# Optimization experiments

Hardware: AMD Instinct MI355X
Metric: run time of the kernel (lower is better)

## Reference

```python
import jax, jax.numpy as jnp
import numpy as np

# Config matching TR_Conv(in_channels=128, out_channels=128, m=5, n=2, dilation=1,
#   concatenate=False -> G_add path, head_paramisloate=False, wide_erf=True, drop=0)
B, C_IN, T = 16, 128, 8192
C_OUT = 128
M, N = 5, 2
ZERO_NUM = 2               # floor(2**(N-1))
UNIT_FZ = 1 + ZERO_NUM     # 3
HEAD = ZERO_NUM            # head_paramisloate=False, zero_num>0 -> head = zero_num
GROUPS = HEAD              # G_add branch: groups = head, Pout_channels = out_channels
KERNEL = UNIT_FZ * (M - 1) + 1  # 13


def quick_gelu(x):
    return x * jax.nn.sigmoid(1.702 * x)


def pad_reflect_to(x, t):
    # TR_Conv.pad_num: reflect-pad last dim up to length t, split (d//2, d-d//2)
    d = t - x.shape[-1]
    if d <= 0:
        return x
    return jnp.pad(x, ((0, 0), (0, 0), (d // 2, d - d // 2)), mode='reflect')


def setup_inputs() -> dict:
    key = jax.random.key(0)
    k1, k2, k3 = jax.random.split(key, 3)
    x = jax.random.normal(k1, (B, C_IN, T), jnp.float32)
    fan_in = (C_IN // GROUPS) * KERNEL
    bound = 1.0 / np.sqrt(fan_in)
    w = jax.random.uniform(k2, (C_OUT, C_IN // GROUPS, KERNEL), jnp.float32, -bound, bound)
    b = jax.random.uniform(k3, (C_OUT,), jnp.float32, -bound, bound)
    return {"x": x, "w": w, "b": b}


def reference(x, w, b):
    t = x.shape[-1]
    # Zero-insertion (UNIT_FZ-1 zeros between samples) + Conv1d(kernel=13, pad=ZERO_NUM,
    # groups=2) expressed exactly via lhs_dilation (equivalent, avoids materializing zeros).
    out = jax.lax.conv_general_dilated(
        x, w, window_strides=(1,), padding=[(ZERO_NUM, ZERO_NUM)],
        lhs_dilation=(UNIT_FZ,), feature_group_count=GROUPS,
        dimension_numbers=('NCH', 'OIH', 'NCH'))  # [B, C_OUT, 3T-10]
    out = out + b[None, :, None]

    # x_m_mk: every UNIT_FZ-th output starting at UNIT_FZ-1, reflect-padded to T
    x_m_mk = pad_reflect_to(out[:, :, UNIT_FZ - 1::UNIT_FZ], t)  # [B, C_OUT, T]

    # wide_erf: sliding max over window M along time, zero-padded (floor/ceil of (M-1)/2)
    lp = (M - 1) // 2
    xp = jnp.pad(x_m_mk, ((0, 0), (0, 0), (lp, M - 1 - lp)))
    umax = jnp.max(jnp.stack([xp[:, :, k:k + t] for k in range(M)], 0), 0)  # [B,C_OUT,T]

    trimmed = out[:, :, :-UNIT_FZ]
    acc = jnp.zeros_like(x_m_mk)
    for j in range(ZERO_NUM):  # all_m=True path: r-l (gelu'd, G_add) and r+l terms
        r = pad_reflect_to(out[:, :, j + UNIT_FZ::UNIT_FZ], t)
        l = pad_reflect_to(trimmed[:, :, j::UNIT_FZ], t)
        minus = quick_gelu(r - l)          # G_add: gelu on the minus branch
        add = r + l
        base = (1.0 / HEAD) * x_m_mk + (1.0 / (2 * HEAD)) * umax  # drop(p=0) = identity
        acc = acc + (minus + base) + (add + base)
    # dilation=1: taylor_eq[:, :, 0::1] = sum over taylor_eq_list[1:]
    return acc
```

## Files before the change

kernel.cpp:

```cpp
#include <hip/hip_runtime.h>
#include <hip/hip_bf16.h>

typedef __attribute__((ext_vector_type(4))) float f32x4;
typedef __attribute__((ext_vector_type(8))) short bf16x8;
typedef unsigned short ushort_t;

#define T_LEN 8192
#define N_REFL 8187
#define TS 64
#define WIN 80
#define XW 88
#define POSTRIDE 66
#define PH_U16 (WIN * POSTRIDE)

__device__ __forceinline__ ushort_t f2bf(float f) {
    union { float f; unsigned u; } a; a.f = f;
    unsigned r = a.u + 0x7FFF + ((a.u >> 16) & 1);
    return (ushort_t)(r >> 16);
}

union bf2u { __hip_bfloat162 h; unsigned u; ushort_t s[2]; };

__device__ __forceinline__ unsigned pack_bf2(float a, float b) {
    bf2u x; x.h = __float22bfloat162_rn(make_float2(a, b));
    return x.u;
}
__device__ __forceinline__ float bflo(unsigned u) {
    union { unsigned u; float f; } x; x.u = u << 16; return x.f;
}
__device__ __forceinline__ float bfhi(unsigned u) {
    union { unsigned u; float f; } x; x.u = u & 0xffff0000u; return x.f;
}
__device__ __forceinline__ float qgelu(float d) {
    return __fdividef(d, 1.f + __expf(-1.702f * d));
}
__device__ __forceinline__ float rot_lane(float v, int byteIdx) {
    int r = __builtin_amdgcn_ds_bpermute(byteIdx, __builtin_bit_cast(int, v));
    return __builtin_bit_cast(float, r);
}

__global__ void convert_w_kernel(const float* __restrict__ w, ushort_t* __restrict__ wbf) {
    int idx = blockIdx.x * 256 + threadIdx.x;
    if (idx >= 128 * 64 * 13) return;
    int tap = idx % 13;
    int c   = (idx / 13) & 63;
    int o   = idx / (13 * 64);
    wbf[(tap * 128 + o) * 64 + c] = f2bf(w[idx]);
}

__global__ __launch_bounds__(256, 4)
void fused_trconv_kernel(const float* __restrict__ x, const ushort_t* __restrict__ wbf,
                         const float* __restrict__ bias, float* __restrict__ out) {
    __shared__ ushort_t smem[3 * PH_U16];
    ushort_t* xs = smem;

    const int bx    = blockIdx.x;
    const int tile  = bx & 127;
    const int g     = (bx >> 7) & 1;
    const int b     = bx >> 8;
    const int t0    = tile * TS;
    const int mbase = t0 - 8;
    const int tid   = threadIdx.x;

    const float* xg = x + ((size_t)b * 128 + (size_t)g * 64) * T_LEN;
    for (int cid = tid; cid < 64 * (XW / 4); cid += 256) {
        int c  = cid & 63;
        int kc = cid >> 6;
        int s0 = kc * 4;
        int m0 = mbase + s0;
        const float* src = xg + (size_t)c * T_LEN + m0;
        float v0, v1, v2, v3;
        if (m0 >= 0 && m0 + 3 < T_LEN) {
            float4 v = *(const float4*)src;
            v0 = v.x; v1 = v.y; v2 = v.z; v3 = v.w;
        } else {
            v0 = (m0 + 0 >= 0 && m0 + 0 < T_LEN) ? src[0] : 0.f;
            v1 = (m0 + 1 >= 0 && m0 + 1 < T_LEN) ? src[1] : 0.f;
            v2 = (m0 + 2 >= 0 && m0 + 2 < T_LEN) ? src[2] : 0.f;
            v3 = (m0 + 3 >= 0 && m0 + 3 < T_LEN) ? src[3] : 0.f;
        }
        unsigned p01 = pack_bf2(v0, v1);
        unsigned p23 = pack_bf2(v2, v3);
        xs[(s0 + 0) * 64 + (c ^ (((s0 + 0) & 7) << 3))] = (ushort_t)(p01 & 0xffff);
        xs[(s0 + 1) * 64 + (c ^ (((s0 + 1) & 7) << 3))] = (ushort_t)(p01 >> 16);
        xs[(s0 + 2) * 64 + (c ^ (((s0 + 2) & 7) << 3))] = (ushort_t)(p23 & 0xffff);
        xs[(s0 + 3) * 64 + (c ^ (((s0 + 3) & 7) << 3))] = (ushort_t)(p23 >> 16);
    }
    __syncthreads();

    const int lane = tid & 63;
    const int wv   = tid >> 6;
    const int row  = lane & 15;
    const int kb   = lane >> 4;

    f32x4 accA[5], accL0[5], accL1[5];
    #pragma unroll
    for (int q = 0; q < 5; ++q) {
        accA[q] = (f32x4){0.f, 0.f, 0.f, 0.f};
        accL0[q] = (f32x4){0.f, 0.f, 0.f, 0.f};
        accL1[q] = (f32x4){0.f, 0.f, 0.f, 0.f};
    }

    const int wo = g * 64 + wv * 16 + row;

    #pragma unroll
    for (int u = 0; u < 5; ++u) {
        #pragma unroll
        for (int h = 0; h < 2; ++h) {
            bf16x8 wf0 = *(const bf16x8*)(wbf + ((3 * u + 0) * 128 + wo) * 64 + h * 32 + kb * 8);
            bf16x8 wf1 = {}, wf2 = {};
            if (u < 4) {
                wf1 = *(const bf16x8*)(wbf + ((3 * u + 2) * 128 + wo) * 64 + h * 32 + kb * 8);
                wf2 = *(const bf16x8*)(wbf + ((3 * u + 1) * 128 + wo) * 64 + h * 32 + kb * 8);
            }
            #pragma unroll
            for (int q = 0; q < 5; ++q) {
                int s = 16 * q + row + u;
                const bf16x8 xa = *(const bf16x8*)(xs + s * 64 + ((h * 32 + kb * 8) ^ ((s & 7) << 3)));
                accA[q] = __builtin_amdgcn_mfma_f32_16x16x32_bf16(xa, wf0, accA[q], 0, 0, 0);
                if (u < 4) {
                    accL0[q] = __builtin_amdgcn_mfma_f32_16x16x32_bf16(xa, wf1, accL0[q], 0, 0, 0);
                    accL1[q] = __builtin_amdgcn_mfma_f32_16x16x32_bf16(xa, wf2, accL1[q], 0, 0, 0);
                }
            }
        }
    }
    const float bo = bias[wo];

    if (tile != 0 && tile != 127) {
        const int upIdx = ((lane + 16) & 63) << 2;
        const int dnIdx = ((lane + 48) & 63) << 2;

        float u0[6], u1[6], d2m[5], d3m[5], lu[6], lv[6];
        #pragma unroll
        for (int q = 0; q < 5; ++q) {
            u0[q] = rot_lane(accA[q][0], upIdx);
            u1[q] = rot_lane(accA[q][1], upIdx);
            d2m[q] = rot_lane(accA[q][2], dnIdx);
            d3m[q] = rot_lane(accA[q][3], dnIdx);
            lu[q] = rot_lane(accL0[q][0], upIdx);
            lv[q] = rot_lane(accL1[q][0], upIdx);
        }
        u0[5] = 0.f; u1[5] = 0.f; lu[5] = 0.f; lv[5] = 0.f;

        const bool kbLT3 = (kb < 3);
        const bool kbGT0 = (kb > 0);
        const float c7bo = 7.f * bo;
        float* outBase = out + ((size_t)(b * 128 + wo)) * T_LEN + (t0 - 6 + 4 * kb);

        #pragma unroll
        for (int q = 0; q < 5; ++q) {
            #pragma unroll
            for (int r = 0; r < 4; ++r) {
                float A0 = accA[q][r];
                float Ap1 = (r < 3) ? accA[q][r + 1] : (kbLT3 ? u0[q] : u0[q + 1]);
                float Ap2 = (r == 0) ? accA[q][2]
                          : (r == 1) ? accA[q][3]
                          : (r == 2) ? (kbLT3 ? u0[q] : u0[q + 1])
                                     : (kbLT3 ? u1[q] : u1[q + 1]);
                float Am1 = (r > 0) ? accA[q][r - 1]
                                    : (kbGT0 ? d3m[q] : (q > 0 ? d3m[q - 1] : 0.f));
                float Am2 = (r == 2) ? accA[q][0]
                          : (r == 3) ? accA[q][1]
                          : (r == 1) ? (kbGT0 ? d3m[q] : (q > 0 ? d3m[q - 1] : 0.f))
                                     : (kbGT0 ? d2m[q] : (q > 0 ? d2m[q - 1] : 0.f));
                float L0a = accL0[q][r];
                float L0b = (r < 3) ? accL0[q][r + 1] : (kbLT3 ? lu[q] : lu[q + 1]);
                float L1a = accL1[q][r];
                float L1b = (r < 3) ? accL1[q][r + 1] : (kbLT3 ? lv[q] : lv[q + 1]);

                float um = fmaxf(fmaxf(fmaxf(Am2, Am1), fmaxf(Ap1, Ap2)), A0);
                float res = 2.f * A0 + um + c7bo + (L0b + L0a) + (L1b + L1a)
                          + qgelu(L0b - L0a) + qgelu(L1b - L1a);

                bool ok = true;
                if (q == 0) ok = (4 * kb + r) >= 6;
                if (q == 4) ok = (4 * kb + r) <= 5;
                if (ok) outBase[16 * q + r] = res;
            }
        }
    } else {
        __syncthreads();
        #pragma unroll
        for (int q = 0; q < 5; ++q) {
            #pragma unroll
            for (int p = 0; p < 3; ++p) {
                const f32x4& a = (p == 0) ? accA[q] : (p == 1) ? accL0[q] : accL1[q];
                unsigned pa = pack_bf2(a[0] + bo, a[1] + bo);
                unsigned pb = pack_bf2(a[2] + bo, a[3] + bo);
                int base = p * PH_U16 + (16 * q + kb * 4) * POSTRIDE + wv * 16 + row;
                smem[base + 0 * POSTRIDE] = (ushort_t)(pa & 0xffff);
                smem[base + 1 * POSTRIDE] = (ushort_t)(pa >> 16);
                smem[base + 2 * POSTRIDE] = (ushort_t)(pb & 0xffff);
                smem[base + 3 * POSTRIDE] = (ushort_t)(pb >> 16);
            }
        }
        __syncthreads();

        const int tl = tid & 63;
        const int wq = tid >> 6;
        const int t  = t0 + tl;
        const ushort_t* phA  = smem;
        const ushort_t* phL0 = smem + PH_U16;
        const ushort_t* phL1 = smem + 2 * PH_U16;
        float* outp = out + ((size_t)b * 128 + (size_t)g * 64) * T_LEN + t;

        int  s5[5];
        bool in5[5];
        #pragma unroll
        for (int dt = 0; dt < 5; ++dt) {
            int tp = t + dt - 2;
            in5[dt] = ((unsigned)tp < (unsigned)T_LEN);
            int idx = tp - 2;
            idx = (idx < 0) ? -idx : idx;
            idx = (idx > N_REFL) ? (2 * N_REFL - idx) : idx;
            s5[dt] = idx - mbase;
        }
        const int sC = s5[2];
        for (int i = 0; i < 8; ++i) {
            int o = 2 * wq + 8 * i;
            unsigned av[5];
            #pragma unroll
            for (int dt = 0; dt < 5; ++dt)
                av[dt] = *(const unsigned*)(phA + s5[dt] * POSTRIDE + o);
            unsigned l0a = *(const unsigned*)(phL0 + (sC    ) * POSTRIDE + o);
            unsigned l0b = *(const unsigned*)(phL0 + (sC + 1) * POSTRIDE + o);
            unsigned l1a = *(const unsigned*)(phL1 + (sC    ) * POSTRIDE + o);
            unsigned l1b = *(const unsigned*)(phL1 + (sC + 1) * POSTRIDE + o);

            float xm_l = bflo(av[2]), xm_h = bfhi(av[2]);
            float um_l = -1e30f, um_h = -1e30f;
            #pragma unroll
            for (int dt = 0; dt < 5; ++dt) {
                um_l = fmaxf(um_l, in5[dt] ? bflo(av[dt]) : 0.f);
                um_h = fmaxf(um_h, in5[dt] ? bfhi(av[dt]) : 0.f);
            }
            float l0al = bflo(l0a), l0bl = bflo(l0b), l1al = bflo(l1a), l1bl = bflo(l1b);
            float l0ah = bfhi(l0a), l0bh = bfhi(l0b), l1ah = bfhi(l1a), l1bh = bfhi(l1b);

            float rl = 2.f * xm_l + um_l + (l0bl + l0al) + qgelu(l0bl - l0al)
                                         + (l1bl + l1al) + qgelu(l1bl - l1al);
            float rh = 2.f * xm_h + um_h + (l0bh + l0ah) + qgelu(l0bh - l0ah)
                                         + (l1bh + l1ah) + qgelu(l1bh - l1ah);
            outp[(size_t)(o    ) * T_LEN] = rl;
            outp[(size_t)(o + 1) * T_LEN] = rh;
        }
    }
}

extern "C" void kernel_launch(void* const* d_in, const int* in_sizes, int n_in,
                              void* d_out, int out_size, void* d_ws, size_t ws_size,
                              hipStream_t stream) {
    const float* x    = (const float*)d_in[0];
    const float* w    = (const float*)d_in[1];
    const float* bias = (const float*)d_in[2];
    float* out        = (float*)d_out;
    ushort_t* wbf     = (ushort_t*)d_ws;

    hipLaunchKernelGGL(convert_w_kernel, dim3(416), dim3(256), 0, stream, w, wbf);
    hipLaunchKernelGGL(fused_trconv_kernel, dim3(16 * 2 * 128), dim3(256), 0, stream,
                       x, wbf, bias, out);
}
```

Baseline: 94.36 us.

## Process four time tiles per block with shared x window, separate edge blocks

Interior blocks now cover 256 time steps: they stage one 288-sample bf16 x window in LDS and then run four 64-step sub-tiles over it. The reflect-boundary tiles move into 64 dedicated blocks at the end of the grid. This cuts the redundant halo loads and the per-block staging and barrier overhead, and removes the edge branch from interior blocks. In exchange the grid shrinks from 4096 to 1088 blocks, occupancy drops to 3 waves per SIMD, and weight fragments are re-read for each sub-tile.

```diff
diff --git a/kernel.cpp b/kernel.cpp
--- a/kernel.cpp
+++ b/kernel.cpp
@@ -7,11 +7,10 @@
 
 #define T_LEN 8192
 #define N_REFL 8187
-#define TS 64
-#define WIN 80
-#define XW 88
+#define GWIN 288
 #define POSTRIDE 66
-#define PH_U16 (WIN * POSTRIDE)
+#define PH_U16 (80 * POSTRIDE)
+#define N_INT 1024
 
 __device__ __forceinline__ ushort_t f2bf(float f) {
     union { float f; unsigned u; } a; a.f = f;
@@ -48,139 +47,213 @@
     wbf[(tap * 128 + o) * 64 + c] = f2bf(w[idx]);
 }
 
-__global__ __launch_bounds__(256, 4)
+__global__ __launch_bounds__(256, 3)
 void fused_trconv_kernel(const float* __restrict__ x, const ushort_t* __restrict__ wbf,
                          const float* __restrict__ bias, float* __restrict__ out) {
-    __shared__ ushort_t smem[3 * PH_U16];
-    ushort_t* xs = smem;
-
-    const int bx    = blockIdx.x;
-    const int tile  = bx & 127;
-    const int g     = (bx >> 7) & 1;
-    const int b     = bx >> 8;
-    const int t0    = tile * TS;
-    const int mbase = t0 - 8;
-    const int tid   = threadIdx.x;
-
-    const float* xg = x + ((size_t)b * 128 + (size_t)g * 64) * T_LEN;
-    for (int cid = tid; cid < 64 * (XW / 4); cid += 256) {
-        int c  = cid & 63;
-        int kc = cid >> 6;
-        int s0 = kc * 4;
-        int m0 = mbase + s0;
-        const float* src = xg + (size_t)c * T_LEN + m0;
-        float v0, v1, v2, v3;
-        if (m0 >= 0 && m0 + 3 < T_LEN) {
-            float4 v = *(const float4*)src;
-            v0 = v.x; v1 = v.y; v2 = v.z; v3 = v.w;
-        } else {
-            v0 = (m0 + 0 >= 0 && m0 + 0 < T_LEN) ? src[0] : 0.f;
-            v1 = (m0 + 1 >= 0 && m0 + 1 < T_LEN) ? src[1] : 0.f;
-            v2 = (m0 + 2 >= 0 && m0 + 2 < T_LEN) ? src[2] : 0.f;
-            v3 = (m0 + 3 >= 0 && m0 + 3 < T_LEN) ? src[3] : 0.f;
-        }
-        unsigned p01 = pack_bf2(v0, v1);
-        unsigned p23 = pack_bf2(v2, v3);
-        xs[(s0 + 0) * 64 + (c ^ (((s0 + 0) & 7) << 3))] = (ushort_t)(p01 & 0xffff);
-        xs[(s0 + 1) * 64 + (c ^ (((s0 + 1) & 7) << 3))] = (ushort_t)(p01 >> 16);
-        xs[(s0 + 2) * 64 + (c ^ (((s0 + 2) & 7) << 3))] = (ushort_t)(p23 & 0xffff);
-        xs[(s0 + 3) * 64 + (c ^ (((s0 + 3) & 7) << 3))] = (ushort_t)(p23 >> 16);
-    }
-    __syncthreads();
-
+    __shared__ ushort_t smem[GWIN * 64];
+
+    const int bx   = blockIdx.x;
+    const int tid  = threadIdx.x;
     const int lane = tid & 63;
     const int wv   = tid >> 6;
     const int row  = lane & 15;
     const int kb   = lane >> 4;
 
-    f32x4 accA[5], accL0[5], accL1[5];
-    #pragma unroll
-    for (int q = 0; q < 5; ++q) {
-        accA[q] = (f32x4){0.f, 0.f, 0.f, 0.f};
-        accL0[q] = (f32x4){0.f, 0.f, 0.f, 0.f};
-        accL1[q] = (f32x4){0.f, 0.f, 0.f, 0.f};
-    }
-
-    const int wo = g * 64 + wv * 16 + row;
-
-    #pragma unroll
-    for (int u = 0; u < 5; ++u) {
-        #pragma unroll
-        for (int h = 0; h < 2; ++h) {
-            bf16x8 wf0 = *(const bf16x8*)(wbf + ((3 * u + 0) * 128 + wo) * 64 + h * 32 + kb * 8);
-            bf16x8 wf1 = {}, wf2 = {};
-            if (u < 4) {
-                wf1 = *(const bf16x8*)(wbf + ((3 * u + 2) * 128 + wo) * 64 + h * 32 + kb * 8);
-                wf2 = *(const bf16x8*)(wbf + ((3 * u + 1) * 128 + wo) * 64 + h * 32 + kb * 8);
-            }
-            #pragma unroll
-            for (int q = 0; q < 5; ++q) {
-                int s = 16 * q + row + u;
-                const bf16x8 xa = *(const bf16x8*)(xs + s * 64 + ((h * 32 + kb * 8) ^ ((s & 7) << 3)));
-                accA[q] = __builtin_amdgcn_mfma_f32_16x16x32_bf16(xa, wf0, accA[q], 0, 0, 0);
-                if (u < 4) {
-                    accL0[q] = __builtin_amdgcn_mfma_f32_16x16x32_bf16(xa, wf1, accL0[q], 0, 0, 0);
-                    accL1[q] = __builtin_amdgcn_mfma_f32_16x16x32_bf16(xa, wf2, accL1[q], 0, 0, 0);
-                }
-            }
-        }
-    }
-    const float bo = bias[wo];
-
-    if (tile != 0 && tile != 127) {
+    if (bx < N_INT) {
+        const int go = bx & 31;
+        const int g  = (bx >> 5) & 1;
+        const int b  = bx >> 6;
+        const int mbase = 256 * go - 8;
+        const float* xg = x + ((size_t)b * 128 + (size_t)g * 64) * T_LEN;
+
+        {
+            const int cl = lane >> 2;
+            const int j  = lane & 3;
+            const int c  = wv * 16 + cl;
+            const float* src = xg + (size_t)c * T_LEN;
+            for (int it = 0; it < 18; ++it) {
+                int m0 = mbase + 16 * it + 4 * j;
+                float v0, v1, v2, v3;
+                if (m0 >= 0 && m0 + 3 < T_LEN) {
+                    float4 v = *(const float4*)(src + m0);
+                    v0 = v.x; v1 = v.y; v2 = v.z; v3 = v.w;
+                } else {
+                    v0 = ((unsigned)(m0 + 0) < (unsigned)T_LEN) ? src[m0 + 0] : 0.f;
+                    v1 = ((unsigned)(m0 + 1) < (unsigned)T_LEN) ? src[m0 + 1] : 0.f;
+                    v2 = ((unsigned)(m0 + 2) < (unsigned)T_LEN) ? src[m0 + 2] : 0.f;
+                    v3 = ((unsigned)(m0 + 3) < (unsigned)T_LEN) ? src[m0 + 3] : 0.f;
+                }
+                unsigned p01 = pack_bf2(v0, v1);
+                unsigned p23 = pack_bf2(v2, v3);
+                int w0 = 16 * it + 4 * j;
+                smem[(w0 + 0) * 64 + (c ^ (((w0 + 0) & 7) << 3))] = (ushort_t)(p01 & 0xffff);
+                smem[(w0 + 1) * 64 + (c ^ (((w0 + 1) & 7) << 3))] = (ushort_t)(p01 >> 16);
+                smem[(w0 + 2) * 64 + (c ^ (((w0 + 2) & 7) << 3))] = (ushort_t)(p23 & 0xffff);
+                smem[(w0 + 3) * 64 + (c ^ (((w0 + 3) & 7) << 3))] = (ushort_t)(p23 >> 16);
+            }
+        }
+        __syncthreads();
+
+        const int wo = g * 64 + wv * 16 + row;
+        const float bo = bias[wo];
+        const float c7bo = 7.f * bo;
         const int upIdx = ((lane + 16) & 63) << 2;
         const int dnIdx = ((lane + 48) & 63) << 2;
-
-        float u0[6], u1[6], d2m[5], d3m[5], lu[6], lv[6];
-        #pragma unroll
-        for (int q = 0; q < 5; ++q) {
-            u0[q] = rot_lane(accA[q][0], upIdx);
-            u1[q] = rot_lane(accA[q][1], upIdx);
-            d2m[q] = rot_lane(accA[q][2], dnIdx);
-            d3m[q] = rot_lane(accA[q][3], dnIdx);
-            lu[q] = rot_lane(accL0[q][0], upIdx);
-            lv[q] = rot_lane(accL1[q][0], upIdx);
-        }
-        u0[5] = 0.f; u1[5] = 0.f; lu[5] = 0.f; lv[5] = 0.f;
-
         const bool kbLT3 = (kb < 3);
         const bool kbGT0 = (kb > 0);
-        const float c7bo = 7.f * bo;
-        float* outBase = out + ((size_t)(b * 128 + wo)) * T_LEN + (t0 - 6 + 4 * kb);
-
+
+        #pragma unroll
+        for (int k = 0; k < 4; ++k) {
+            if ((go == 0 && k == 0) || (go == 31 && k == 3)) continue;
+            if (k) asm volatile("" ::: "memory");
+
+            f32x4 accA[5], accL0[5], accL1[5];
+            #pragma unroll
+            for (int q = 0; q < 5; ++q) {
+                accA[q]  = (f32x4){0.f, 0.f, 0.f, 0.f};
+                accL0[q] = (f32x4){0.f, 0.f, 0.f, 0.f};
+                accL1[q] = (f32x4){0.f, 0.f, 0.f, 0.f};
+            }
+
+            #pragma unroll
+            for (int u = 0; u < 5; ++u) {
+                #pragma unroll
+                for (int h = 0; h < 2; ++h) {
+                    bf16x8 wf0 = *(const bf16x8*)(wbf + ((3 * u + 0) * 128 + wo) * 64 + h * 32 + kb * 8);
+                    bf16x8 wf1 = {}, wf2 = {};
+                    if (u < 4) {
+                        wf1 = *(const bf16x8*)(wbf + ((3 * u + 2) * 128 + wo) * 64 + h * 32 + kb * 8);
+                        wf2 = *(const bf16x8*)(wbf + ((3 * u + 1) * 128 + wo) * 64 + h * 32 + kb * 8);
+                    }
+                    #pragma unroll
+                    for (int q = 0; q < 5; ++q) {
+                        int s = 64 * k + 16 * q + row + u;
+                        const bf16x8 xa = *(const bf16x8*)(smem + s * 64 + ((h * 32 + kb * 8) ^ ((s & 7) << 3)));
+                        accA[q] = __builtin_amdgcn_mfma_f32_16x16x32_bf16(xa, wf0, accA[q], 0, 0, 0);
+                        if (u < 4) {
+                            accL0[q] = __builtin_amdgcn_mfma_f32_16x16x32_bf16(xa, wf1, accL0[q], 0, 0, 0);
+                            accL1[q] = __builtin_amdgcn_mfma_f32_16x16x32_bf16(xa, wf2, accL1[q], 0, 0, 0);
+                        }
+                    }
+                }
+            }
+
+            float u0[6], u1[6], d2m[5], d3m[5], lu[6], lv[6];
+            #pragma unroll
+            for (int q = 0; q < 5; ++q) {
+                u0[q]  = rot_lane(accA[q][0], upIdx);
+                u1[q]  = rot_lane(accA[q][1], upIdx);
+                d2m[q] = rot_lane(accA[q][2], dnIdx);
+                d3m[q] = rot_lane(accA[q][3], dnIdx);
+                lu[q]  = rot_lane(accL0[q][0], upIdx);
+                lv[q]  = rot_lane(accL1[q][0], upIdx);
+            }
+            u0[5] = 0.f; u1[5] = 0.f; lu[5] = 0.f; lv[5] = 0.f;
+
+            const int t0k = 256 * go + 64 * k;
+            float* outBase = out + ((size_t)(b * 128 + wo)) * T_LEN + (t0k - 6 + 4 * kb);
+
+            #pragma unroll
+            for (int q = 0; q < 5; ++q) {
+                #pragma unroll
+                for (int r = 0; r < 4; ++r) {
+                    float A0 = accA[q][r];
+                    float Ap1 = (r < 3) ? accA[q][r + 1] : (kbLT3 ? u0[q] : u0[q + 1]);
+                    float Ap2 = (r == 0) ? accA[q][2]
+                              : (r == 1) ? accA[q][3]
+                              : (r == 2) ? (kbLT3 ? u0[q] : u0[q + 1])
+                                         : (kbLT3 ? u1[q] : u1[q + 1]);
+                    float Am1 = (r > 0) ? accA[q][r - 1]
+                                        : (kbGT0 ? d3m[q] : (q > 0 ? d3m[q - 1] : 0.f));
+                    float Am2 = (r == 2) ? accA[q][0]
+                              : (r == 3) ? accA[q][1]
+                              : (r == 1) ? (kbGT0 ? d3m[q] : (q > 0 ? d3m[q - 1] : 0.f))
+                                         : (kbGT0 ? d2m[q] : (q > 0 ? d2m[q - 1] : 0.f));
+                    float L0a = accL0[q][r];
+                    float L0b = (r < 3) ? accL0[q][r + 1] : (kbLT3 ? lu[q] : lu[q + 1]);
+                    float L1a = accL1[q][r];
+                    float L1b = (r < 3) ? accL1[q][r + 1] : (kbLT3 ? lv[q] : lv[q + 1]);
+
+                    float um = fmaxf(fmaxf(fmaxf(Am2, Am1), fmaxf(Ap1, Ap2)), A0);
+                    float res = 2.f * A0 + um + c7bo + (L0b + L0a) + (L1b + L1a)
+                              + qgelu(L0b - L0a) + qgelu(L1b - L1a);
+
+                    bool ok = true;
+                    if (q == 0) ok = (4 * kb + r) >= 6;
+                    if (q == 4) ok = (4 * kb + r) <= 5;
+                    if (ok) outBase[16 * q + r] = res;
+                }
+            }
+        }
+    } else {
+        const int idx  = bx - N_INT;
+        const int tile = (idx & 1) ? 127 : 0;
+        const int g    = (idx >> 1) & 1;
+        const int b    = idx >> 2;
+        const int t0    = tile * 64;
+        const int mbase = t0 - 8;
+        ushort_t* xs = smem;
+
+        const float* xg = x + ((size_t)b * 128 + (size_t)g * 64) * T_LEN;
+        for (int cid = tid; cid < 64 * 22; cid += 256) {
+            int c  = cid & 63;
+            int kc = cid >> 6;
+            int s0 = kc * 4;
+            int m0 = mbase + s0;
+            const float* src = xg + (size_t)c * T_LEN + m0;
+            float v0, v1, v2, v3;
+            if (m0 >= 0 && m0 + 3 < T_LEN) {
+                float4 v = *(const float4*)src;
+                v0 = v.x; v1 = v.y; v2 = v.z; v3 = v.w;
+            } else {
+                v0 = (m0 + 0 >= 0 && m0 + 0 < T_LEN) ? src[0] : 0.f;
+                v1 = (m0 + 1 >= 0 && m0 + 1 < T_LEN) ? src[1] : 0.f;
+                v2 = (m0 + 2 >= 0 && m0 + 2 < T_LEN) ? src[2] : 0.f;
+                v3 = (m0 + 3 >= 0 && m0 + 3 < T_LEN) ? src[3] : 0.f;
+            }
+            unsigned p01 = pack_bf2(v0, v1);
+            unsigned p23 = pack_bf2(v2, v3);
+            xs[(s0 + 0) * 64 + (c ^ (((s0 + 0) & 7) << 3))] = (ushort_t)(p01 & 0xffff);
+            xs[(s0 + 1) * 64 + (c ^ (((s0 + 1) & 7) << 3))] = (ushort_t)(p01 >> 16);
+            xs[(s0 + 2) * 64 + (c ^ (((s0 + 2) & 7) << 3))] = (ushort_t)(p23 & 0xffff);
+            xs[(s0 + 3) * 64 + (c ^ (((s0 + 3) & 7) << 3))] = (ushort_t)(p23 >> 16);
+        }
+        __syncthreads();
+
+        f32x4 accA[5], accL0[5], accL1[5];
         #pragma unroll
         for (int q = 0; q < 5; ++q) {
-            #pragma unroll
-            for (int r = 0; r < 4; ++r) {
-                float A0 = accA[q][r];
-                float Ap1 = (r < 3) ? accA[q][r + 1] : (kbLT3 ? u0[q] : u0[q + 1]);
-                float Ap2 = (r == 0) ? accA[q][2]
-                          : (r == 1) ? accA[q][3]
-                          : (r == 2) ? (kbLT3 ? u0[q] : u0[q + 1])
-                                     : (kbLT3 ? u1[q] : u1[q + 1]);
-                float Am1 = (r > 0) ? accA[q][r - 1]
-                                    : (kbGT0 ? d3m[q] : (q > 0 ? d3m[q - 1] : 0.f));
-                float Am2 = (r == 2) ? accA[q][0]
-                          : (r == 3) ? accA[q][1]
-                          : (r == 1) ? (kbGT0 ? d3m[q] : (q > 0 ? d3m[q - 1] : 0.f))
-                                     : (kbGT0 ? d2m[q] : (q > 0 ? d2m[q - 1] : 0.f));
-                float L0a = accL0[q][r];
-                float L0b = (r < 3) ? accL0[q][r + 1] : (kbLT3 ? lu[q] : lu[q + 1]);
-                float L1a = accL1[q][r];
-                float L1b = (r < 3) ? accL1[q][r + 1] : (kbLT3 ? lv[q] : lv[q + 1]);
-
-                float um = fmaxf(fmaxf(fmaxf(Am2, Am1), fmaxf(Ap1, Ap2)), A0);
-                float res = 2.f * A0 + um + c7bo + (L0b + L0a) + (L1b + L1a)
-                          + qgelu(L0b - L0a) + qgelu(L1b - L1a);
-
-                bool ok = true;
-                if (q == 0) ok = (4 * kb + r) >= 6;
-                if (q == 4) ok = (4 * kb + r) <= 5;
-                if (ok) outBase[16 * q + r] = res;
-            }
-        }
-    } else {
+            accA[q]  = (f32x4){0.f, 0.f, 0.f, 0.f};
+            accL0[q] = (f32x4){0.f, 0.f, 0.f, 0.f};
+            accL1[q] = (f32x4){0.f, 0.f, 0.f, 0.f};
+        }
+        const int wo = g * 64 + wv * 16 + row;
+
+        #pragma unroll
+        for (int u = 0; u < 5; ++u) {
+            #pragma unroll
+            for (int h = 0; h < 2; ++h) {
+                bf16x8 wf0 = *(const bf16x8*)(wbf + ((3 * u + 0) * 128 + wo) * 64 + h * 32 + kb * 8);
+                bf16x8 wf1 = {}, wf2 = {};
+                if (u < 4) {
+                    wf1 = *(const bf16x8*)(wbf + ((3 * u + 2) * 128 + wo) * 64 + h * 32 + kb * 8);
+                    wf2 = *(const bf16x8*)(wbf + ((3 * u + 1) * 128 + wo) * 64 + h * 32 + kb * 8);
+                }
+                #pragma unroll
+                for (int q = 0; q < 5; ++q) {
+                    int s = 16 * q + row + u;
+                    const bf16x8 xa = *(const bf16x8*)(xs + s * 64 + ((h * 32 + kb * 8) ^ ((s & 7) << 3)));
+                    accA[q] = __builtin_amdgcn_mfma_f32_16x16x32_bf16(xa, wf0, accA[q], 0, 0, 0);
+                    if (u < 4) {
+                        accL0[q] = __builtin_amdgcn_mfma_f32_16x16x32_bf16(xa, wf1, accL0[q], 0, 0, 0);
+                        accL1[q] = __builtin_amdgcn_mfma_f32_16x16x32_bf16(xa, wf2, accL1[q], 0, 0, 0);
+                    }
+                }
+            }
+        }
+        const float bo = bias[wo];
         __syncthreads();
+
         #pragma unroll
         for (int q = 0; q < 5; ++q) {
             #pragma unroll
@@ -211,10 +284,10 @@
         for (int dt = 0; dt < 5; ++dt) {
             int tp = t + dt - 2;
             in5[dt] = ((unsigned)tp < (unsigned)T_LEN);
-            int idx = tp - 2;
-            idx = (idx < 0) ? -idx : idx;
-            idx = (idx > N_REFL) ? (2 * N_REFL - idx) : idx;
-            s5[dt] = idx - mbase;
+            int ix = tp - 2;
+            ix = (ix < 0) ? -ix : ix;
+            ix = (ix > N_REFL) ? (2 * N_REFL - ix) : ix;
+            s5[dt] = ix - mbase;
         }
         const int sC = s5[2];
         for (int i = 0; i < 8; ++i) {
@@ -258,6 +331,6 @@
     ushort_t* wbf     = (ushort_t*)d_ws;
 
     hipLaunchKernelGGL(convert_w_kernel, dim3(416), dim3(256), 0, stream, w, wbf);
-    hipLaunchKernelGGL(fused_trconv_kernel, dim3(16 * 2 * 128), dim3(256), 0, stream,
+    hipLaunchKernelGGL(fused_trconv_kernel, dim3(N_INT + 64), dim3(256), 0, stream,
                        x, wbf, bias, out);
 }
```

Result: slower. 97.50 us (+3.3%).

## Fold neighbor-sum/difference into combined weights and split interior/boundary kernels

Applied to the files above, without the earlier changes.

Interior tiles now use precomputed combined weights so the MFMAs directly produce A, the full sum term (2A+L0+L0'+L1+L1'), and the two differences fed to quick_gelu. This removes the lane rotations and extra adds for the L terms in the epilogue, at the cost of four MFMA streams per tap instead of roughly three. Boundary tiles move to a separate small kernel, which removes branching from the interior kernel. The interior qgelu also switches to exp2 with a reciprocal.

```diff
diff --git a/kernel.cpp b/kernel.cpp
--- a/kernel.cpp
+++ b/kernel.cpp
@@ -7,11 +7,10 @@
 
 #define T_LEN 8192
 #define N_REFL 8187
-#define TS 64
-#define WIN 80
-#define XW 88
 #define POSTRIDE 66
-#define PH_U16 (WIN * POSTRIDE)
+#define PH_U16 (80 * POSTRIDE)
+#define N_INT 4032
+#define WS_WNEW_OFF 262144
 
 __device__ __forceinline__ ushort_t f2bf(float f) {
     union { float f; unsigned u; } a; a.f = f;
@@ -32,6 +31,9 @@
     union { unsigned u; float f; } x; x.u = u & 0xffff0000u; return x.f;
 }
 __device__ __forceinline__ float qgelu(float d) {
+    return d * __frcp_rn(1.f + exp2f(-2.4553418f * d));
+}
+__device__ __forceinline__ float qgelu2(float d) {
     return __fdividef(d, 1.f + __expf(-1.702f * d));
 }
 __device__ __forceinline__ float rot_lane(float v, int byteIdx) {
@@ -39,34 +41,166 @@
     return __builtin_bit_cast(float, r);
 }
 
-__global__ void convert_w_kernel(const float* __restrict__ w, ushort_t* __restrict__ wbf) {
+__global__ void convert_w_kernel(const float* __restrict__ w,
+                                 ushort_t* __restrict__ wold,
+                                 ushort_t* __restrict__ wnew) {
     int idx = blockIdx.x * 256 + threadIdx.x;
-    if (idx >= 128 * 64 * 13) return;
-    int tap = idx % 13;
-    int c   = (idx / 13) & 63;
-    int o   = idx / (13 * 64);
-    wbf[(tap * 128 + o) * 64 + c] = f2bf(w[idx]);
+    if (idx >= 8192) return;
+    int o = idx >> 6, c = idx & 63;
+    const float* wp = w + (size_t)idx * 13;
+    float t[13];
+    #pragma unroll
+    for (int k = 0; k < 13; ++k) t[k] = wp[k];
+    #pragma unroll
+    for (int k = 0; k < 13; ++k) wold[(k * 128 + o) * 64 + c] = f2bf(t[k]);
+    #pragma unroll
+    for (int k = 0; k < 5; ++k) {
+        float a   = t[3 * k];
+        float l0k = (k <= 3) ? t[3 * k + 2] : 0.f;
+        float l1k = (k <= 3) ? t[3 * k + 1] : 0.f;
+        float l0m = (k >= 1) ? t[3 * k - 1] : 0.f;
+        float l1m = (k >= 1) ? t[3 * k - 2] : 0.f;
+        wnew[((0 * 5 + k) * 128 + o) * 64 + c] = f2bf(a);
+        wnew[((1 * 5 + k) * 128 + o) * 64 + c] = f2bf(2.f * a + l0k + l0m + l1k + l1m);
+        wnew[((2 * 5 + k) * 128 + o) * 64 + c] = f2bf(l0m - l0k);
+        wnew[((3 * 5 + k) * 128 + o) * 64 + c] = f2bf(l1m - l1k);
+    }
+}
+
+__global__ __launch_bounds__(256, 3)
+void fused_int_kernel(const float* __restrict__ x, const ushort_t* __restrict__ wnew,
+                      const float* __restrict__ bias, float* __restrict__ out) {
+    __shared__ ushort_t xs[88 * 64];
+
+    const int bx   = blockIdx.x;
+    const int tid  = threadIdx.x;
+    const int lane = tid & 63;
+    const int wv   = tid >> 6;
+    const int row  = lane & 15;
+    const int kb   = lane >> 4;
+
+    const int gb   = bx / 126;
+    const int tile = 1 + (bx - gb * 126);
+    const int g    = gb & 1;
+    const int b    = gb >> 1;
+    const int t0   = tile * 64;
+    const int mbase = t0 - 8;
+
+    const float* xg = x + ((size_t)b * 128 + (size_t)g * 64) * T_LEN;
+    for (int cid = tid; cid < 64 * 22; cid += 256) {
+        int c  = cid & 63;
+        int s0 = (cid >> 6) * 4;
+        float4 v = *(const float4*)(xg + (size_t)c * T_LEN + (mbase + s0));
+        unsigned p01 = pack_bf2(v.x, v.y);
+        unsigned p23 = pack_bf2(v.z, v.w);
+        xs[(s0 + 0) * 64 + (c ^ (((s0 + 0) & 7) << 3))] = (ushort_t)(p01 & 0xffff);
+        xs[(s0 + 1) * 64 + (c ^ (((s0 + 1) & 7) << 3))] = (ushort_t)(p01 >> 16);
+        xs[(s0 + 2) * 64 + (c ^ (((s0 + 2) & 7) << 3))] = (ushort_t)(p23 & 0xffff);
+        xs[(s0 + 3) * 64 + (c ^ (((s0 + 3) & 7) << 3))] = (ushort_t)(p23 >> 16);
+    }
+    const int wo = g * 64 + wv * 16 + row;
+    const float bo = bias[wo];
+    __syncthreads();
+
+    f32x4 accA[5], accS[5], accD0[5], accD1[5];
+    #pragma unroll
+    for (int q = 0; q < 5; ++q) {
+        accA[q]  = (f32x4){0.f, 0.f, 0.f, 0.f};
+        accS[q]  = (f32x4){0.f, 0.f, 0.f, 0.f};
+        accD0[q] = (f32x4){0.f, 0.f, 0.f, 0.f};
+        accD1[q] = (f32x4){0.f, 0.f, 0.f, 0.f};
+    }
+
+    #pragma unroll
+    for (int u = 0; u < 5; ++u) {
+        #pragma unroll
+        for (int h = 0; h < 2; ++h) {
+            const int wbase = h * 32 + kb * 8;
+            bf16x8 wfA = *(const bf16x8*)(wnew + ((0 * 5 + u) * 128 + wo) * 64 + wbase);
+            bf16x8 wfS = *(const bf16x8*)(wnew + ((1 * 5 + u) * 128 + wo) * 64 + wbase);
+            bf16x8 wf0 = *(const bf16x8*)(wnew + ((2 * 5 + u) * 128 + wo) * 64 + wbase);
+            bf16x8 wf1 = *(const bf16x8*)(wnew + ((3 * 5 + u) * 128 + wo) * 64 + wbase);
+            #pragma unroll
+            for (int q = 0; q < 5; ++q) {
+                int s = 16 * q + row + u;
+                const bf16x8 xa = *(const bf16x8*)(xs + s * 64 + (wbase ^ ((s & 7) << 3)));
+                accA[q]  = __builtin_amdgcn_mfma_f32_16x16x32_bf16(xa, wfA, accA[q],  0, 0, 0);
+                accS[q]  = __builtin_amdgcn_mfma_f32_16x16x32_bf16(xa, wfS, accS[q],  0, 0, 0);
+                accD0[q] = __builtin_amdgcn_mfma_f32_16x16x32_bf16(xa, wf0, accD0[q], 0, 0, 0);
+                accD1[q] = __builtin_amdgcn_mfma_f32_16x16x32_bf16(xa, wf1, accD1[q], 0, 0, 0);
+            }
+        }
+    }
+
+    const int upIdx = ((lane + 16) & 63) << 2;
+    const int dnIdx = ((lane + 48) & 63) << 2;
+
+    float u0[6], u1[6], d2m[5], d3m[5];
+    #pragma unroll
+    for (int q = 0; q < 5; ++q) {
+        u0[q]  = rot_lane(accA[q][0], upIdx);
+        u1[q]  = rot_lane(accA[q][1], upIdx);
+        d2m[q] = rot_lane(accA[q][2], dnIdx);
+        d3m[q] = rot_lane(accA[q][3], dnIdx);
+    }
+    u0[5] = 0.f; u1[5] = 0.f;
+
+    const bool kbLT3 = (kb < 3);
+    const bool kbGT0 = (kb > 0);
+    const float c7bo = 7.f * bo;
+    float* outBase = out + ((size_t)(b * 128 + wo)) * T_LEN + (t0 - 6 + 4 * kb);
+
+    #pragma unroll
+    for (int q = 0; q < 5; ++q) {
+        #pragma unroll
+        for (int r = 0; r < 4; ++r) {
+            float A0 = accA[q][r];
+            float Ap1 = (r < 3) ? accA[q][r + 1] : (kbLT3 ? u0[q] : u0[q + 1]);
+            float Ap2 = (r == 0) ? accA[q][2]
+                      : (r == 1) ? accA[q][3]
+                      : (r == 2) ? (kbLT3 ? u0[q] : u0[q + 1])
+                                 : (kbLT3 ? u1[q] : u1[q + 1]);
+            float Am1 = (r > 0) ? accA[q][r - 1]
+                                : (kbGT0 ? d3m[q] : (q > 0 ? d3m[q - 1] : 0.f));
+            float Am2 = (r == 2) ? accA[q][0]
+                      : (r == 3) ? accA[q][1]
+                      : (r == 1) ? (kbGT0 ? d3m[q] : (q > 0 ? d3m[q - 1] : 0.f))
+                                 : (kbGT0 ? d2m[q] : (q > 0 ? d2m[q - 1] : 0.f));
+
+            float um  = fmaxf(fmaxf(fmaxf(Am2, Am1), A0), fmaxf(Ap1, Ap2));
+            float res = accS[q][r] + um + c7bo + qgelu(accD0[q][r]) + qgelu(accD1[q][r]);
+
+            bool ok = true;
+            if (q == 0) ok = (4 * kb + r) >= 6;
+            if (q == 4) ok = (4 * kb + r) <= 5;
+            if (ok) outBase[16 * q + r] = res;
+        }
+    }
 }
 
 __global__ __launch_bounds__(256, 4)
-void fused_trconv_kernel(const float* __restrict__ x, const ushort_t* __restrict__ wbf,
-                         const float* __restrict__ bias, float* __restrict__ out) {
+void fused_bnd_kernel(const float* __restrict__ x, const ushort_t* __restrict__ wbf,
+                      const float* __restrict__ bias, float* __restrict__ out) {
     __shared__ ushort_t smem[3 * PH_U16];
     ushort_t* xs = smem;
 
-    const int bx    = blockIdx.x;
-    const int tile  = bx & 127;
-    const int g     = (bx >> 7) & 1;
-    const int b     = bx >> 8;
-    const int t0    = tile * TS;
+    const int idx  = blockIdx.x;
+    const int tid  = threadIdx.x;
+    const int lane = tid & 63;
+    const int wv   = tid >> 6;
+    const int row  = lane & 15;
+    const int kb   = lane >> 4;
+
+    const int tile = (idx & 1) ? 127 : 0;
+    const int g    = (idx >> 1) & 1;
+    const int b    = idx >> 2;
+    const int t0    = tile * 64;
     const int mbase = t0 - 8;
-    const int tid   = threadIdx.x;
 
     const float* xg = x + ((size_t)b * 128 + (size_t)g * 64) * T_LEN;
-    for (int cid = tid; cid < 64 * (XW / 4); cid += 256) {
+    for (int cid = tid; cid < 64 * 22; cid += 256) {
         int c  = cid & 63;
-        int kc = cid >> 6;
-        int s0 = kc * 4;
+        int s0 = (cid >> 6) * 4;
         int m0 = mbase + s0;
         const float* src = xg + (size_t)c * T_LEN + m0;
         float v0, v1, v2, v3;
@@ -74,10 +208,10 @@
             float4 v = *(const float4*)src;
             v0 = v.x; v1 = v.y; v2 = v.z; v3 = v.w;
         } else {
-            v0 = (m0 + 0 >= 0 && m0 + 0 < T_LEN) ? src[0] : 0.f;
-            v1 = (m0 + 1 >= 0 && m0 + 1 < T_LEN) ? src[1] : 0.f;
-            v2 = (m0 + 2 >= 0 && m0 + 2 < T_LEN) ? src[2] : 0.f;
-            v3 = (m0 + 3 >= 0 && m0 + 3 < T_LEN) ? src[3] : 0.f;
+            v0 = ((unsigned)(m0 + 0) < (unsigned)T_LEN) ? src[0] : 0.f;
+            v1 = ((unsigned)(m0 + 1) < (unsigned)T_LEN) ? src[1] : 0.f;
+            v2 = ((unsigned)(m0 + 2) < (unsigned)T_LEN) ? src[2] : 0.f;
+            v3 = ((unsigned)(m0 + 3) < (unsigned)T_LEN) ? src[3] : 0.f;
         }
         unsigned p01 = pack_bf2(v0, v1);
         unsigned p23 = pack_bf2(v2, v3);
@@ -88,19 +222,13 @@
     }
     __syncthreads();
 
-    const int lane = tid & 63;
-    const int wv   = tid >> 6;
-    const int row  = lane & 15;
-    const int kb   = lane >> 4;
-
     f32x4 accA[5], accL0[5], accL1[5];
     #pragma unroll
     for (int q = 0; q < 5; ++q) {
-        accA[q] = (f32x4){0.f, 0.f, 0.f, 0.f};
+        accA[q]  = (f32x4){0.f, 0.f, 0.f, 0.f};
         accL0[q] = (f32x4){0.f, 0.f, 0.f, 0.f};
         accL1[q] = (f32x4){0.f, 0.f, 0.f, 0.f};
     }
-
     const int wo = g * 64 + wv * 16 + row;
 
     #pragma unroll
@@ -126,125 +254,71 @@
         }
     }
     const float bo = bias[wo];
-
-    if (tile != 0 && tile != 127) {
-        const int upIdx = ((lane + 16) & 63) << 2;
-        const int dnIdx = ((lane + 48) & 63) << 2;
-
-        float u0[6], u1[6], d2m[5], d3m[5], lu[6], lv[6];
-        #pragma unroll
-        for (int q = 0; q < 5; ++q) {
-            u0[q] = rot_lane(accA[q][0], upIdx);
-            u1[q] = rot_lane(accA[q][1], upIdx);
-            d2m[q] = rot_lane(accA[q][2], dnIdx);
-            d3m[q] = rot_lane(accA[q][3], dnIdx);
-            lu[q] = rot_lane(accL0[q][0], upIdx);
-            lv[q] = rot_lane(accL1[q][0], upIdx);
-        }
-        u0[5] = 0.f; u1[5] = 0.f; lu[5] = 0.f; lv[5] = 0.f;
-
-        const bool kbLT3 = (kb < 3);
-        const bool kbGT0 = (kb > 0);
-        const float c7bo = 7.f * bo;
-        float* outBase = out + ((size_t)(b * 128 + wo)) * T_LEN + (t0 - 6 + 4 * kb);
-
-        #pragma unroll
-        for (int q = 0; q < 5; ++q) {
-            #pragma unroll
-            for (int r = 0; r < 4; ++r) {
-                float A0 = accA[q][r];
-                float Ap1 = (r < 3) ? accA[q][r + 1] : (kbLT3 ? u0[q] : u0[q + 1]);
-                float Ap2 = (r == 0) ? accA[q][2]
-                          : (r == 1) ? accA[q][3]
-                          : (r == 2) ? (kbLT3 ? u0[q] : u0[q + 1])
-                                     : (kbLT3 ? u1[q] : u1[q + 1]);
-                float Am1 = (r > 0) ? accA[q][r - 1]
-                                    : (kbGT0 ? d3m[q] : (q > 0 ? d3m[q - 1] : 0.f));
-                float Am2 = (r == 2) ? accA[q][0]
-                          : (r == 3) ? accA[q][1]
-                          : (r == 1) ? (kbGT0 ? d3m[q] : (q > 0 ? d3m[q - 1] : 0.f))
-                                     : (kbGT0 ? d2m[q] : (q > 0 ? d2m[q - 1] : 0.f));
-                float L0a = accL0[q][r];
-                float L0b = (r < 3) ? accL0[q][r + 1] : (kbLT3 ? lu[q] : lu[q + 1]);
-                float L1a = accL1[q][r];
-                float L1b = (r < 3) ? accL1[q][r + 1] : (kbLT3 ? lv[q] : lv[q + 1]);
-
-                float um = fmaxf(fmaxf(fmaxf(Am2, Am1), fmaxf(Ap1, Ap2)), A0);
-                float res = 2.f * A0 + um + c7bo + (L0b + L0a) + (L1b + L1a)
-                          + qgelu(L0b - L0a) + qgelu(L1b - L1a);
-
-                bool ok = true;
-                if (q == 0) ok = (4 * kb + r) >= 6;
-                if (q == 4) ok = (4 * kb + r) <= 5;
-                if (ok) outBase[16 * q + r] = res;
-            }
-        }
-    } else {
-        __syncthreads();
-        #pragma unroll
-        for (int q = 0; q < 5; ++q) {
-            #pragma unroll
-            for (int p = 0; p < 3; ++p) {
-                const f32x4& a = (p == 0) ? accA[q] : (p == 1) ? accL0[q] : accL1[q];
-                unsigned pa = pack_bf2(a[0] + bo, a[1] + bo);
-                unsigned pb = pack_bf2(a[2] + bo, a[3] + bo);
-                int base = p * PH_U16 + (16 * q + kb * 4) * POSTRIDE + wv * 16 + row;
-                smem[base + 0 * POSTRIDE] = (ushort_t)(pa & 0xffff);
-                smem[base + 1 * POSTRIDE] = (ushort_t)(pa >> 16);
-                smem[base + 2 * POSTRIDE] = (ushort_t)(pb & 0xffff);
-                smem[base + 3 * POSTRIDE] = (ushort_t)(pb >> 16);
-            }
-        }
-        __syncthreads();
-
-        const int tl = tid & 63;
-        const int wq = tid >> 6;
-        const int t  = t0 + tl;
-        const ushort_t* phA  = smem;
-        const ushort_t* phL0 = smem + PH_U16;
-        const ushort_t* phL1 = smem + 2 * PH_U16;
-        float* outp = out + ((size_t)b * 128 + (size_t)g * 64) * T_LEN + t;
-
-        int  s5[5];
-        bool in5[5];
+    __syncthreads();
+
+    #pragma unroll
+    for (int q = 0; q < 5; ++q) {
+        #pragma unroll
+        for (int p = 0; p < 3; ++p) {
+            const f32x4& a = (p == 0) ? accA[q] : (p == 1) ? accL0[q] : accL1[q];
+            unsigned pa = pack_bf2(a[0] + bo, a[1] + bo);
+            unsigned pb = pack_bf2(a[2] + bo, a[3] + bo);
+            int base = p * PH_U16 + (16 * q + kb * 4) * POSTRIDE + wv * 16 + row;
+            smem[base + 0 * POSTRIDE] = (ushort_t)(pa & 0xffff);
+            smem[base + 1 * POSTRIDE] = (ushort_t)(pa >> 16);
+            smem[base + 2 * POSTRIDE] = (ushort_t)(pb & 0xffff);
+            smem[base + 3 * POSTRIDE] = (ushort_t)(pb >> 16);
+        }
+    }
+    __syncthreads();
+
+    const int tl = tid & 63;
+    const int wq = tid >> 6;
+    const int t  = t0 + tl;
+    const ushort_t* phA  = smem;
+    const ushort_t* phL0 = smem + PH_U16;
+    const ushort_t* phL1 = smem + 2 * PH_U16;
+    float* outp = out + ((size_t)b * 128 + (size_t)g * 64) * T_LEN + t;
+
+    int  s5[5];
+    bool in5[5];
+    #pragma unroll
+    for (int dt = 0; dt < 5; ++dt) {
+        int tp = t + dt - 2;
+        in5[dt] = ((unsigned)tp < (unsigned)T_LEN);
+        int ix = tp - 2;
+        ix = (ix < 0) ? -ix : ix;
+        ix = (ix > N_REFL) ? (2 * N_REFL - ix) : ix;
+        s5[dt] = ix - mbase;
+    }
+    const int sC = s5[2];
+    for (int i = 0; i < 8; ++i) {
+        int o = 2 * wq + 8 * i;
+        unsigned av[5];
+        #pragma unroll
+        for (int dt = 0; dt < 5; ++dt)
+            av[dt] = *(const unsigned*)(phA + s5[dt] * POSTRIDE + o);
+        unsigned l0a = *(const unsigned*)(phL0 + (sC    ) * POSTRIDE + o);
+        unsigned l0b = *(const unsigned*)(phL0 + (sC + 1) * POSTRIDE + o);
+        unsigned l1a = *(const unsigned*)(phL1 + (sC    ) * POSTRIDE + o);
+        unsigned l1b = *(const unsigned*)(phL1 + (sC + 1) * POSTRIDE + o);
+
+        float xm_l = bflo(av[2]), xm_h = bfhi(av[2]);
+        float um_l = -1e30f, um_h = -1e30f;
         #pragma unroll
         for (int dt = 0; dt < 5; ++dt) {
-            int tp = t + dt - 2;
-            in5[dt] = ((unsigned)tp < (unsigned)T_LEN);
-            int idx = tp - 2;
-            idx = (idx < 0) ? -idx : idx;
-            idx = (idx > N_REFL) ? (2 * N_REFL - idx) : idx;
-            s5[dt] = idx - mbase;
-        }
-        const int sC = s5[2];
-        for (int i = 0; i < 8; ++i) {
-            int o = 2 * wq + 8 * i;
-            unsigned av[5];
-            #pragma unroll
-            for (int dt = 0; dt < 5; ++dt)
-                av[dt] = *(const unsigned*)(phA + s5[dt] * POSTRIDE + o);
-            unsigned l0a = *(const unsigned*)(phL0 + (sC    ) * POSTRIDE + o);
-            unsigned l0b = *(const unsigned*)(phL0 + (sC + 1) * POSTRIDE + o);
-            unsigned l1a = *(const unsigned*)(phL1 + (sC    ) * POSTRIDE + o);
-            unsigned l1b = *(const unsigned*)(phL1 + (sC + 1) * POSTRIDE + o);
-
-            float xm_l = bflo(av[2]), xm_h = bfhi(av[2]);
-            float um_l = -1e30f, um_h = -1e30f;
-            #pragma unroll
-            for (int dt = 0; dt < 5; ++dt) {
-                um_l = fmaxf(um_l, in5[dt] ? bflo(av[dt]) : 0.f);
-                um_h = fmaxf(um_h, in5[dt] ? bfhi(av[dt]) : 0.f);
-            }
-            float l0al = bflo(l0a), l0bl = bflo(l0b), l1al = bflo(l1a), l1bl = bflo(l1b);
-            float l0ah = bfhi(l0a), l0bh = bfhi(l0b), l1ah = bfhi(l1a), l1bh = bfhi(l1b);
-
-            float rl = 2.f * xm_l + um_l + (l0bl + l0al) + qgelu(l0bl - l0al)
-                                         + (l1bl + l1al) + qgelu(l1bl - l1al);
-            float rh = 2.f * xm_h + um_h + (l0bh + l0ah) + qgelu(l0bh - l0ah)
-                                         + (l1bh + l1ah) + qgelu(l1bh - l1ah);
-            outp[(size_t)(o    ) * T_LEN] = rl;
-            outp[(size_t)(o + 1) * T_LEN] = rh;
-        }
+            um_l = fmaxf(um_l, in5[dt] ? bflo(av[dt]) : 0.f);
+            um_h = fmaxf(um_h, in5[dt] ? bfhi(av[dt]) : 0.f);
+        }
+        float l0al = bflo(l0a), l0bl = bflo(l0b), l1al = bflo(l1a), l1bl = bflo(l1b);
+        float l0ah = bfhi(l0a), l0bh = bfhi(l0b), l1ah = bfhi(l1a), l1bh = bfhi(l1b);
+
+        float rl = 2.f * xm_l + um_l + (l0bl + l0al) + qgelu2(l0bl - l0al)
+                                     + (l1bl + l1al) + qgelu2(l1bl - l1al);
+        float rh = 2.f * xm_h + um_h + (l0bh + l0ah) + qgelu2(l0bh - l0ah)
+                                     + (l1bh + l1ah) + qgelu2(l1bh - l1ah);
+        outp[(size_t)(o    ) * T_LEN] = rl;
+        outp[(size_t)(o + 1) * T_LEN] = rh;
     }
 }
 
@@ -255,9 +329,12 @@
     const float* w    = (const float*)d_in[1];
     const float* bias = (const float*)d_in[2];
     float* out        = (float*)d_out;
-    ushort_t* wbf     = (ushort_t*)d_ws;
-
-    hipLaunchKernelGGL(convert_w_kernel, dim3(416), dim3(256), 0, stream, w, wbf);
-    hipLaunchKernelGGL(fused_trconv_kernel, dim3(16 * 2 * 128), dim3(256), 0, stream,
-                       x, wbf, bias, out);
-}
+    ushort_t* wold    = (ushort_t*)d_ws;
+    ushort_t* wnew    = (ushort_t*)((char*)d_ws + WS_WNEW_OFF);
+
+    hipLaunchKernelGGL(convert_w_kernel, dim3(32), dim3(256), 0, stream, w, wold, wnew);
+    hipLaunchKernelGGL(fused_int_kernel, dim3(N_INT), dim3(256), 0, stream,
+                       x, wnew, bias, out);
+    hipLaunchKernelGGL(fused_bnd_kernel, dim3(64), dim3(256), 0, stream,
+                       x, wold, bias, out);
+}
```

After: 125.6 us. 1.33x slower.
